# Kernel optimization log

Hardware: AMD Instinct MI355X
Metric: run time of the kernel (lower is better)

The kernel has to match this reference:

```python
import jax, jax.numpy as jnp
import numpy as np

HID = 5120
NH = 40
HD = HID // NH  # 128
S = 2048        # q_len == model_max_length (prefill)


def setup_inputs() -> dict:
    key = jax.random.key(0)
    k1, k2, k3 = jax.random.split(key, 3)
    hidden_states = jax.random.normal(k1, (1, S, HID), dtype=jnp.float32)
    W_pack_w = jax.random.normal(k2, (3 * HID, HID), dtype=jnp.float32) * 0.02
    o_proj_w = jax.random.normal(k3, (HID, HID), dtype=jnp.float32) * 0.02
    k_cache = jnp.zeros((1, NH, S, HD), dtype=jnp.float32)
    v_cache = jnp.zeros((1, NH, S, HD), dtype=jnp.float32)
    input_pos = jnp.arange(S, dtype=jnp.int32)
    # persistent causal mask [bsz, 1, max_len, max_len]; True = attend
    attention_mask = jnp.tril(jnp.ones((S, S), dtype=bool))[None, None, :, :]
    return {
        "hidden_states": hidden_states,
        "W_pack_w": W_pack_w,
        "o_proj_w": o_proj_w,
        "k_cache": k_cache,
        "v_cache": v_cache,
        "input_pos": input_pos,
        "attention_mask": attention_mask,
    }


def reference(hidden_states, W_pack_w, o_proj_w, k_cache, v_cache, input_pos, attention_mask):
    bsz, q_len, _ = hidden_states.shape
    # fused QKV projection (torch Linear weight is [out, in])
    proj = jnp.einsum("bsh,oh->bso", hidden_states, W_pack_w)  # [1,S,3H]
    q, k, v = jnp.split(proj, 3, axis=-1)
    def to_heads(t):
        return t.reshape(bsz, q_len, NH, HD).transpose(0, 2, 1, 3)  # [1,NH,S,HD]
    q, k, v = to_heads(q), to_heads(k), to_heads(v)
    # KV-cache scatter update at input_pos
    k_cache = k_cache.at[:, :, input_pos, :].set(k)
    v_cache = v_cache.at[:, :, input_pos, :].set(v)
    # s_len = input_pos[-1] + 1 == S (full prefill, static shape)
    keys = k_cache  # [1,NH,S,HD]
    vals = v_cache
    mask = attention_mask[:, :, input_pos, :]  # [1,1,S,S]
    scale = 1.0 / jnp.sqrt(jnp.asarray(HD, dtype=q.dtype))
    scores = jnp.einsum("bhqd,bhkd->bhqk", q, keys) * scale  # [1,NH,S,S]
    neg = jnp.finfo(scores.dtype).min
    scores = jnp.where(mask, scores, neg)
    attn = jax.nn.softmax(scores, axis=-1)
    out = jnp.einsum("bhqk,bhkd->bhqd", attn, vals)  # [1,NH,S,HD]
    out = out.transpose(0, 2, 1, 3).reshape(bsz, q_len, HID)
    return jnp.einsum("bsh,oh->bso", out, o_proj_w)
```

## Files before the change

kernel.cpp:

```cpp
#include <hip/hip_runtime.h>

#define S 2048
#define HID 5120
#define NH 40
#define HD 128

typedef unsigned short u16;
typedef __attribute__((ext_vector_type(8))) short short8;
typedef __attribute__((ext_vector_type(4))) float f32x4;

__device__ __forceinline__ u16 f2bf(float f) {
  union { float f; unsigned u; } x; x.f = f;
  unsigned r = x.u + 0x7fffu + ((x.u >> 16) & 1u);
  return (u16)(r >> 16);
}

__device__ __forceinline__ void gl_lds16(const void* g, void* l) {
  __builtin_amdgcn_global_load_lds((__attribute__((address_space(1))) void*)g,
                                   (__attribute__((address_space(3))) void*)l,
                                   16, 0, 0);
}

__global__ __launch_bounds__(256) void cvt4(const float4* __restrict__ s,
                                            ushort4* __restrict__ d, int n4) {
  int i = blockIdx.x * 256 + threadIdx.x;
  if (i >= n4) return;
  float4 v = s[i];
  ushort4 o;
  o.x = f2bf(v.x); o.y = f2bf(v.y); o.z = f2bf(v.z); o.w = f2bf(v.w);
  d[i] = o;
}

__global__ __launch_bounds__(256) void gemm_bt(
    const u16* __restrict__ A, const u16* __restrict__ B,
    int N, int K,
    float* __restrict__ C,
    u16* __restrict__ qb, u16* __restrict__ kb, u16* __restrict__ vtb,
    int mode)
{
  __shared__ __align__(16) u16 As[128 * 64];
  __shared__ __align__(16) u16 Bs[128 * 64];
  const int tid = threadIdx.x;
  const int lane = tid & 63;
  const int wid = tid >> 6;
  const int wm = wid >> 1, wn = wid & 1;
  const int l16 = lane & 15, quad = lane >> 4;
  const int m0 = blockIdx.x * 128, n0 = blockIdx.y * 128;

  f32x4 acc[4][4];
#pragma unroll
  for (int i = 0; i < 4; ++i)
#pragma unroll
    for (int j = 0; j < 4; ++j)
      acc[i][j] = (f32x4){0.f, 0.f, 0.f, 0.f};

  const int srow = lane >> 3;
  const int scb = lane & 7;

  for (int k0 = 0; k0 < K; k0 += 64) {
#pragma unroll
    for (int cc = 0; cc < 4; ++cc) {
      int c = wid * 4 + cc;
      int row = c * 8 + srow;
      int cb = scb ^ (row & 7);
      gl_lds16(A + (long)(m0 + row) * K + k0 + cb * 8, &As[c * 512]);
    }
#pragma unroll
    for (int cc = 0; cc < 4; ++cc) {
      int c = wid * 4 + cc;
      int row = c * 8 + srow;
      int cb = scb ^ (row & 7);
      gl_lds16(B + (long)(n0 + row) * K + k0 + cb * 8, &Bs[c * 512]);
    }
    __syncthreads();
#pragma unroll
    for (int kk = 0; kk < 64; kk += 32) {
      short8 af[4], bg[4];
      const int cb0 = (kk >> 3) + quad;
#pragma unroll
      for (int i = 0; i < 4; ++i) {
        int row = wm * 64 + i * 16 + l16;
        af[i] = *(const short8*)&As[row * 64 + (cb0 ^ (row & 7)) * 8];
      }
#pragma unroll
      for (int j = 0; j < 4; ++j) {
        int row = wn * 64 + j * 16 + l16;
        bg[j] = *(const short8*)&Bs[row * 64 + (cb0 ^ (row & 7)) * 8];
      }
#pragma unroll
      for (int i = 0; i < 4; ++i)
#pragma unroll
        for (int j = 0; j < 4; ++j)
          acc[i][j] = __builtin_amdgcn_mfma_f32_16x16x32_bf16(af[i], bg[j], acc[i][j], 0, 0, 0);
    }
    __syncthreads();
  }

  if (mode == 0) {
#pragma unroll
    for (int i = 0; i < 4; ++i)
#pragma unroll
      for (int r = 0; r < 4; ++r) {
        int row = m0 + wm * 64 + i * 16 + quad * 4 + r;
#pragma unroll
        for (int j = 0; j < 4; ++j) {
          int col = n0 + wn * 64 + j * 16 + l16;
          C[(long)row * N + col] = acc[i][j][r];
        }
      }
  } else {
    const int which = n0 / HID;
    const int head = (n0 % HID) >> 7;
    const float qs = 0.08838834764831845f;
#pragma unroll
    for (int i = 0; i < 4; ++i)
#pragma unroll
      for (int j = 0; j < 4; ++j)
#pragma unroll
        for (int r = 0; r < 4; ++r) {
          int sI = m0 + wm * 64 + i * 16 + quad * 4 + r;
          int d = wn * 64 + j * 16 + l16;
          float v = acc[i][j][r];
          if (which == 0)      qb[((long)head * S + sI) * HD + d] = f2bf(v * qs);
          else if (which == 1) kb[((long)head * S + sI) * HD + d] = f2bf(v);
          else                 vtb[((long)head * HD + d) * S + sI] = f2bf(v);
        }
  }
}

__global__ __launch_bounds__(256) void attn_kernel(
    const u16* __restrict__ qg, const u16* __restrict__ kg,
    const u16* __restrict__ vg, u16* __restrict__ og)
{
  __shared__ __align__(16) u16 Qs[64 * 128];
  __shared__ __align__(16) u16 Ks[64 * 128];
  __shared__ __align__(16) u16 Vs[128 * 64];
  __shared__ float redm[2][64];
  __shared__ float reds[2][64];

  const int tid = threadIdx.x;
  const int lane = tid & 63;
  const int wid = tid >> 6;
  const int wm = wid >> 1, wn = wid & 1;
  const int l16 = lane & 15, quad = lane >> 4;
  const int qt = blockIdx.x;
  const int h = blockIdx.y;
  const int q0 = qt * 64;

  u16* Ps = Ks;

  {
    const u16* src = qg + ((long)h * S + q0) * HD;
#pragma unroll
    for (int cc = 0; cc < 4; ++cc) {
      int c = wid * 4 + cc;
      int row = c * 4 + (lane >> 4);
      int cb = (lane & 15) ^ (row & 7);
      gl_lds16(src + row * HD + cb * 8, &Qs[c * 512]);
    }
  }

  f32x4 acc_o[2][4];
#pragma unroll
  for (int i = 0; i < 2; ++i)
#pragma unroll
    for (int j = 0; j < 4; ++j)
      acc_o[i][j] = (f32x4){0.f, 0.f, 0.f, 0.f};
  float m_st[2][4], l_st[2][4];
#pragma unroll
  for (int i = 0; i < 2; ++i)
#pragma unroll
    for (int r = 0; r < 4; ++r) { m_st[i][r] = -1e30f; l_st[i][r] = 0.f; }

  for (int kt = 0; kt <= qt; ++kt) {
    __syncthreads();
    {
      const u16* ksrc = kg + ((long)h * S + kt * 64) * HD;
#pragma unroll
      for (int cc = 0; cc < 4; ++cc) {
        int c = wid * 4 + cc;
        int row = c * 4 + (lane >> 4);
        int cb = (lane & 15) ^ (row & 7);
        gl_lds16(ksrc + row * HD + cb * 8, &Ks[c * 512]);
      }
      const u16* vsrc = vg + (long)h * HD * S + kt * 64;
#pragma unroll
      for (int cc = 0; cc < 4; ++cc) {
        int c = wid * 4 + cc;
        int row = c * 8 + (lane >> 3);
        int cb = (lane & 7) ^ (row & 7);
        gl_lds16(vsrc + (long)row * S + cb * 8, &Vs[c * 512]);
      }
    }
    __syncthreads();

    f32x4 acc_s[2][2];
#pragma unroll
    for (int i = 0; i < 2; ++i)
#pragma unroll
      for (int j = 0; j < 2; ++j)
        acc_s[i][j] = (f32x4){0.f, 0.f, 0.f, 0.f};
#pragma unroll
    for (int kk = 0; kk < 128; kk += 32) {
      short8 aq[2], bk[2];
      const int cb0 = (kk >> 3) + quad;
#pragma unroll
      for (int i = 0; i < 2; ++i) {
        int row = wm * 32 + i * 16 + l16;
        aq[i] = *(const short8*)&Qs[row * 128 + (cb0 ^ (row & 7)) * 8];
      }
#pragma unroll
      for (int j = 0; j < 2; ++j) {
        int row = wn * 32 + j * 16 + l16;
        bk[j] = *(const short8*)&Ks[row * 128 + (cb0 ^ (row & 7)) * 8];
      }
#pragma unroll
      for (int i = 0; i < 2; ++i)
#pragma unroll
        for (int j = 0; j < 2; ++j)
          acc_s[i][j] = __builtin_amdgcn_mfma_f32_16x16x32_bf16(aq[i], bk[j], acc_s[i][j], 0, 0, 0);
    }

    if (kt == qt) {
#pragma unroll
      for (int i = 0; i < 2; ++i)
#pragma unroll
        for (int j = 0; j < 2; ++j)
#pragma unroll
          for (int r = 0; r < 4; ++r) {
            int row = wm * 32 + i * 16 + quad * 4 + r;
            int col = wn * 32 + j * 16 + l16;
            if (col > row) acc_s[i][j][r] = -1e30f;
          }
    }

#pragma unroll
    for (int i = 0; i < 2; ++i)
#pragma unroll
      for (int r = 0; r < 4; ++r) {
        float v = fmaxf(acc_s[i][0][r], acc_s[i][1][r]);
        v = fmaxf(v, __shfl_xor(v, 1));
        v = fmaxf(v, __shfl_xor(v, 2));
        v = fmaxf(v, __shfl_xor(v, 4));
        v = fmaxf(v, __shfl_xor(v, 8));
        if (l16 == 0) redm[wn][wm * 32 + i * 16 + quad * 4 + r] = v;
      }
    __syncthreads();

    float alpha[2][4], mnew[2][4], psum[2][4];
#pragma unroll
    for (int i = 0; i < 2; ++i)
#pragma unroll
      for (int r = 0; r < 4; ++r) {
        int row = wm * 32 + i * 16 + quad * 4 + r;
        float mn = fmaxf(m_st[i][r], fmaxf(redm[0][row], redm[1][row]));
        mnew[i][r] = mn;
        alpha[i][r] = __expf(m_st[i][r] - mn);
        m_st[i][r] = mn;
        psum[i][r] = 0.f;
      }
#pragma unroll
    for (int i = 0; i < 2; ++i)
#pragma unroll
      for (int j = 0; j < 2; ++j)
#pragma unroll
        for (int r = 0; r < 4; ++r) {
          int row = wm * 32 + i * 16 + quad * 4 + r;
          int col = wn * 32 + j * 16 + l16;
          float p = __expf(acc_s[i][j][r] - mnew[i][r]);
          psum[i][r] += p;
          Ps[row * 64 + ((col >> 3) ^ (row & 7)) * 8 + (col & 7)] = f2bf(p);
        }
#pragma unroll
    for (int i = 0; i < 2; ++i)
#pragma unroll
      for (int r = 0; r < 4; ++r) {
        float v = psum[i][r];
        v += __shfl_xor(v, 1);
        v += __shfl_xor(v, 2);
        v += __shfl_xor(v, 4);
        v += __shfl_xor(v, 8);
        if (l16 == 0) reds[wn][wm * 32 + i * 16 + quad * 4 + r] = v;
      }
    __syncthreads();

#pragma unroll
    for (int i = 0; i < 2; ++i)
#pragma unroll
      for (int r = 0; r < 4; ++r) {
        int row = wm * 32 + i * 16 + quad * 4 + r;
        l_st[i][r] = alpha[i][r] * l_st[i][r] + reds[0][row] + reds[1][row];
#pragma unroll
        for (int j = 0; j < 4; ++j)
          acc_o[i][j][r] *= alpha[i][r];
      }
#pragma unroll
    for (int kk = 0; kk < 64; kk += 32) {
      short8 ap[2], bv[4];
      const int cb0 = (kk >> 3) + quad;
#pragma unroll
      for (int i = 0; i < 2; ++i) {
        int m = wm * 32 + i * 16 + l16;
        ap[i] = *(const short8*)&Ps[m * 64 + (cb0 ^ (m & 7)) * 8];
      }
#pragma unroll
      for (int j = 0; j < 4; ++j) {
        int n = wn * 64 + j * 16 + l16;
        bv[j] = *(const short8*)&Vs[n * 64 + (cb0 ^ (n & 7)) * 8];
      }
#pragma unroll
      for (int i = 0; i < 2; ++i)
#pragma unroll
        for (int j = 0; j < 4; ++j)
          acc_o[i][j] = __builtin_amdgcn_mfma_f32_16x16x32_bf16(ap[i], bv[j], acc_o[i][j], 0, 0, 0);
    }
  }

#pragma unroll
  for (int i = 0; i < 2; ++i)
#pragma unroll
    for (int r = 0; r < 4; ++r) {
      int row = wm * 32 + i * 16 + quad * 4 + r;
      float inv = 1.f / l_st[i][r];
#pragma unroll
      for (int j = 0; j < 4; ++j) {
        int d = wn * 64 + j * 16 + l16;
        og[(long)(q0 + row) * HID + h * HD + d] = f2bf(acc_o[i][j][r] * inv);
      }
    }
}

extern "C" void kernel_launch(void* const* d_in, const int* in_sizes, int n_in,
                              void* d_out, int out_size, void* d_ws, size_t ws_size,
                              hipStream_t stream) {
  const float* hs = (const float*)d_in[0];
  const float* wp = (const float*)d_in[1];
  const float* wo = (const float*)d_in[2];
  float* out = (float*)d_out;
  char* ws = (char*)d_ws;

  u16* hsb = (u16*)(ws);
  u16* wpb = (u16*)(ws + 20971520L);
  u16* wob = (u16*)(ws + 178257920L);
  u16* qb  = (u16*)(ws + 230686720L);
  u16* kb  = (u16*)(ws + 251658240L);
  u16* vtb = (u16*)(ws + 272629760L);
  u16* aob = (u16*)(ws + 293601280L);
  if (ws_size < 314572800UL) return;

  cvt4<<<10240, 256, 0, stream>>>((const float4*)hs, (ushort4*)hsb, 2621440);
  cvt4<<<76800, 256, 0, stream>>>((const float4*)wp, (ushort4*)wpb, 19660800);
  cvt4<<<25600, 256, 0, stream>>>((const float4*)wo, (ushort4*)wob, 6553600);

  gemm_bt<<<dim3(16, 120), 256, 0, stream>>>(hsb, wpb, 15360, 5120,
                                             nullptr, qb, kb, vtb, 1);
  attn_kernel<<<dim3(32, 40), 256, 0, stream>>>(qb, kb, vtb, aob);
  gemm_bt<<<dim3(16, 40), 256, 0, stream>>>(aob, wob, 5120, 5120,
                                            out, nullptr, nullptr, nullptr, 0);
}
```

Before: 1.651 ms.

## Restructure attention so each wave owns 32 query rows, dropping LDS staging and barriers

The attention kernel now gives each wave an independent 32-row query strip within a 128-row block. Q is held in registers, and K/V fragments are read straight from global memory instead of being staged through shared LDS tiles. This removes every __syncthreads and the cross-wave max/sum reductions through LDS; only a per-wave P buffer stays in LDS. The grid is halved and issued in reverse order so heavy causal blocks start first, with launch bounds set to allow 2 blocks per CU. The cost is extra global/L2 traffic, since K and V are no longer shared across waves, plus higher register pressure from the 2x8 output accumulators and the Q fragments.

```diff
diff --git a/kernel.cpp b/kernel.cpp
--- a/kernel.cpp
+++ b/kernel.cpp
@@ -128,43 +128,35 @@
   }
 }
 
-__global__ __launch_bounds__(256) void attn_kernel(
+__global__ __launch_bounds__(256, 2) void attn_kernel(
     const u16* __restrict__ qg, const u16* __restrict__ kg,
     const u16* __restrict__ vg, u16* __restrict__ og)
 {
-  __shared__ __align__(16) u16 Qs[64 * 128];
-  __shared__ __align__(16) u16 Ks[64 * 128];
-  __shared__ __align__(16) u16 Vs[128 * 64];
-  __shared__ float redm[2][64];
-  __shared__ float reds[2][64];
+  __shared__ __align__(16) u16 Ps[4][32 * 64];
 
   const int tid = threadIdx.x;
   const int lane = tid & 63;
   const int wid = tid >> 6;
-  const int wm = wid >> 1, wn = wid & 1;
   const int l16 = lane & 15, quad = lane >> 4;
-  const int qt = blockIdx.x;
+  const int bq = 15 - blockIdx.x;
   const int h = blockIdx.y;
-  const int q0 = qt * 64;
-
-  u16* Ps = Ks;
-
-  {
-    const u16* src = qg + ((long)h * S + q0) * HD;
-#pragma unroll
-    for (int cc = 0; cc < 4; ++cc) {
-      int c = wid * 4 + cc;
-      int row = c * 4 + (lane >> 4);
-      int cb = (lane & 15) ^ (row & 7);
-      gl_lds16(src + row * HD + cb * 8, &Qs[c * 512]);
-    }
-  }
-
-  f32x4 acc_o[2][4];
+  const int q0 = bq * 128 + wid * 32;
+
+  u16* P = &Ps[wid][0];
+
+  short8 qf[2][4];
 #pragma unroll
   for (int i = 0; i < 2; ++i)
 #pragma unroll
-    for (int j = 0; j < 4; ++j)
+    for (int kk = 0; kk < 4; ++kk)
+      qf[i][kk] = *(const short8*)(qg + ((long)h * S + q0 + i * 16 + l16) * HD
+                                   + kk * 32 + quad * 8);
+
+  f32x4 acc_o[2][8];
+#pragma unroll
+  for (int i = 0; i < 2; ++i)
+#pragma unroll
+    for (int j = 0; j < 8; ++j)
       acc_o[i][j] = (f32x4){0.f, 0.f, 0.f, 0.f};
   float m_st[2][4], l_st[2][4];
 #pragma unroll
@@ -172,105 +164,76 @@
 #pragma unroll
     for (int r = 0; r < 4; ++r) { m_st[i][r] = -1e30f; l_st[i][r] = 0.f; }
 
-  for (int kt = 0; kt <= qt; ++kt) {
-    __syncthreads();
-    {
-      const u16* ksrc = kg + ((long)h * S + kt * 64) * HD;
-#pragma unroll
-      for (int cc = 0; cc < 4; ++cc) {
-        int c = wid * 4 + cc;
-        int row = c * 4 + (lane >> 4);
-        int cb = (lane & 15) ^ (row & 7);
-        gl_lds16(ksrc + row * HD + cb * 8, &Ks[c * 512]);
-      }
-      const u16* vsrc = vg + (long)h * HD * S + kt * 64;
-#pragma unroll
-      for (int cc = 0; cc < 4; ++cc) {
-        int c = wid * 4 + cc;
-        int row = c * 8 + (lane >> 3);
-        int cb = (lane & 7) ^ (row & 7);
-        gl_lds16(vsrc + (long)row * S + cb * 8, &Vs[c * 512]);
-      }
-    }
-    __syncthreads();
-
-    f32x4 acc_s[2][2];
+  const int nkt = (q0 + 32 + 63) >> 6;
+
+  for (int kt = 0; kt < nkt; ++kt) {
+    f32x4 acc_s[2][4];
 #pragma unroll
     for (int i = 0; i < 2; ++i)
 #pragma unroll
-      for (int j = 0; j < 2; ++j)
+      for (int j = 0; j < 4; ++j)
         acc_s[i][j] = (f32x4){0.f, 0.f, 0.f, 0.f};
-#pragma unroll
-    for (int kk = 0; kk < 128; kk += 32) {
-      short8 aq[2], bk[2];
-      const int cb0 = (kk >> 3) + quad;
-#pragma unroll
-      for (int i = 0; i < 2; ++i) {
-        int row = wm * 32 + i * 16 + l16;
-        aq[i] = *(const short8*)&Qs[row * 128 + (cb0 ^ (row & 7)) * 8];
-      }
-#pragma unroll
-      for (int j = 0; j < 2; ++j) {
-        int row = wn * 32 + j * 16 + l16;
-        bk[j] = *(const short8*)&Ks[row * 128 + (cb0 ^ (row & 7)) * 8];
-      }
+
+    short8 kf[4][4];
+#pragma unroll
+    for (int j = 0; j < 4; ++j)
+#pragma unroll
+      for (int kk = 0; kk < 4; ++kk)
+        kf[j][kk] = *(const short8*)(kg + ((long)h * S + kt * 64 + j * 16 + l16) * HD
+                                     + kk * 32 + quad * 8);
+#pragma unroll
+    for (int kk = 0; kk < 4; ++kk)
 #pragma unroll
       for (int i = 0; i < 2; ++i)
 #pragma unroll
-        for (int j = 0; j < 2; ++j)
-          acc_s[i][j] = __builtin_amdgcn_mfma_f32_16x16x32_bf16(aq[i], bk[j], acc_s[i][j], 0, 0, 0);
-    }
-
-    if (kt == qt) {
+        for (int j = 0; j < 4; ++j)
+          acc_s[i][j] = __builtin_amdgcn_mfma_f32_16x16x32_bf16(qf[i][kk], kf[j][kk],
+                                                                acc_s[i][j], 0, 0, 0);
+
+    if (kt == nkt - 1) {
 #pragma unroll
       for (int i = 0; i < 2; ++i)
 #pragma unroll
-        for (int j = 0; j < 2; ++j)
+        for (int j = 0; j < 4; ++j)
 #pragma unroll
           for (int r = 0; r < 4; ++r) {
-            int row = wm * 32 + i * 16 + quad * 4 + r;
-            int col = wn * 32 + j * 16 + l16;
+            int row = q0 + i * 16 + quad * 4 + r;
+            int col = kt * 64 + j * 16 + l16;
             if (col > row) acc_s[i][j][r] = -1e30f;
           }
     }
 
+    float alpha[2][4], mnew[2][4], psum[2][4];
 #pragma unroll
     for (int i = 0; i < 2; ++i)
 #pragma unroll
       for (int r = 0; r < 4; ++r) {
-        float v = fmaxf(acc_s[i][0][r], acc_s[i][1][r]);
+        float v = fmaxf(fmaxf(acc_s[i][0][r], acc_s[i][1][r]),
+                        fmaxf(acc_s[i][2][r], acc_s[i][3][r]));
         v = fmaxf(v, __shfl_xor(v, 1));
         v = fmaxf(v, __shfl_xor(v, 2));
         v = fmaxf(v, __shfl_xor(v, 4));
         v = fmaxf(v, __shfl_xor(v, 8));
-        if (l16 == 0) redm[wn][wm * 32 + i * 16 + quad * 4 + r] = v;
-      }
-    __syncthreads();
-
-    float alpha[2][4], mnew[2][4], psum[2][4];
-#pragma unroll
-    for (int i = 0; i < 2; ++i)
-#pragma unroll
-      for (int r = 0; r < 4; ++r) {
-        int row = wm * 32 + i * 16 + quad * 4 + r;
-        float mn = fmaxf(m_st[i][r], fmaxf(redm[0][row], redm[1][row]));
+        float mn = fmaxf(m_st[i][r], v);
         mnew[i][r] = mn;
         alpha[i][r] = __expf(m_st[i][r] - mn);
         m_st[i][r] = mn;
         psum[i][r] = 0.f;
       }
+
 #pragma unroll
     for (int i = 0; i < 2; ++i)
 #pragma unroll
-      for (int j = 0; j < 2; ++j)
+      for (int j = 0; j < 4; ++j)
 #pragma unroll
         for (int r = 0; r < 4; ++r) {
-          int row = wm * 32 + i * 16 + quad * 4 + r;
-          int col = wn * 32 + j * 16 + l16;
+          int lr = i * 16 + quad * 4 + r;
+          int lc = j * 16 + l16;
           float p = __expf(acc_s[i][j][r] - mnew[i][r]);
           psum[i][r] += p;
-          Ps[row * 64 + ((col >> 3) ^ (row & 7)) * 8 + (col & 7)] = f2bf(p);
+          P[lr * 64 + (((lc >> 3) ^ (lr & 7)) << 3) + (lc & 7)] = f2bf(p);
         }
+
 #pragma unroll
     for (int i = 0; i < 2; ++i)
 #pragma unroll
@@ -280,39 +243,30 @@
         v += __shfl_xor(v, 2);
         v += __shfl_xor(v, 4);
         v += __shfl_xor(v, 8);
-        if (l16 == 0) reds[wn][wm * 32 + i * 16 + quad * 4 + r] = v;
-      }
-    __syncthreads();
-
-#pragma unroll
-    for (int i = 0; i < 2; ++i)
-#pragma unroll
-      for (int r = 0; r < 4; ++r) {
-        int row = wm * 32 + i * 16 + quad * 4 + r;
-        l_st[i][r] = alpha[i][r] * l_st[i][r] + reds[0][row] + reds[1][row];
-#pragma unroll
-        for (int j = 0; j < 4; ++j)
+        l_st[i][r] = alpha[i][r] * l_st[i][r] + v;
+#pragma unroll
+        for (int j = 0; j < 8; ++j)
           acc_o[i][j][r] *= alpha[i][r];
       }
+
 #pragma unroll
     for (int kk = 0; kk < 64; kk += 32) {
-      short8 ap[2], bv[4];
+      short8 ap[2];
       const int cb0 = (kk >> 3) + quad;
 #pragma unroll
       for (int i = 0; i < 2; ++i) {
-        int m = wm * 32 + i * 16 + l16;
-        ap[i] = *(const short8*)&Ps[m * 64 + (cb0 ^ (m & 7)) * 8];
-      }
-#pragma unroll
-      for (int j = 0; j < 4; ++j) {
-        int n = wn * 64 + j * 16 + l16;
-        bv[j] = *(const short8*)&Vs[n * 64 + (cb0 ^ (n & 7)) * 8];
-      }
-#pragma unroll
-      for (int i = 0; i < 2; ++i)
-#pragma unroll
-        for (int j = 0; j < 4; ++j)
-          acc_o[i][j] = __builtin_amdgcn_mfma_f32_16x16x32_bf16(ap[i], bv[j], acc_o[i][j], 0, 0, 0);
+        int m = i * 16 + l16;
+        ap[i] = *(const short8*)&P[m * 64 + ((cb0 ^ (m & 7)) << 3)];
+      }
+#pragma unroll
+      for (int j = 0; j < 8; ++j) {
+        short8 bv = *(const short8*)(vg + ((long)h * HD + j * 16 + l16) * S
+                                     + kt * 64 + kk + quad * 8);
+#pragma unroll
+        for (int i = 0; i < 2; ++i)
+          acc_o[i][j] = __builtin_amdgcn_mfma_f32_16x16x32_bf16(ap[i], bv,
+                                                                acc_o[i][j], 0, 0, 0);
+      }
     }
   }
 
@@ -320,12 +274,12 @@
   for (int i = 0; i < 2; ++i)
 #pragma unroll
     for (int r = 0; r < 4; ++r) {
-      int row = wm * 32 + i * 16 + quad * 4 + r;
       float inv = 1.f / l_st[i][r];
-#pragma unroll
-      for (int j = 0; j < 4; ++j) {
-        int d = wn * 64 + j * 16 + l16;
-        og[(long)(q0 + row) * HID + h * HD + d] = f2bf(acc_o[i][j][r] * inv);
+      int row = q0 + i * 16 + quad * 4 + r;
+#pragma unroll
+      for (int j = 0; j < 8; ++j) {
+        int d = j * 16 + l16;
+        og[(long)row * HID + h * HD + d] = f2bf(acc_o[i][j][r] * inv);
       }
     }
 }
@@ -354,7 +308,7 @@
 
   gemm_bt<<<dim3(16, 120), 256, 0, stream>>>(hsb, wpb, 15360, 5120,
                                              nullptr, qb, kb, vtb, 1);
-  attn_kernel<<<dim3(32, 40), 256, 0, stream>>>(qb, kb, vtb, aob);
+  attn_kernel<<<dim3(16, 40), 256, 0, stream>>>(qb, kb, vtb, aob);
   gemm_bt<<<dim3(16, 40), 256, 0, stream>>>(aob, wob, 5120, 5120,
                                             out, nullptr, nullptr, nullptr, 0);
 }
```

Measured after the change: 1.755 ms. 6.3% more time.
